# Performance work log

Measured on AMD Instinct MI355X. Metric: run time of the kernel, lower is better.

The kernel has to match this reference:

```python
import jax, jax.numpy as jnp
import numpy as np

N_FEAT = 8   # node_features_count
E_FEAT = 4   # edge_features_count
NUM_IN = 2 * (N_FEAT + 2) + E_FEAT + 1   # 25
NUM_OUT = 2 * N_FEAT + E_FEAT           # 20
E = 1048576  # number of edges (batched)


def setup_inputs() -> dict:
    key = jax.random.key(0)
    ks = jax.random.split(key, 12)
    inp = {
        "r": jax.random.uniform(ks[0], (E,), dtype=jnp.float32),
        "a_data": jax.random.normal(ks[1], (E, N_FEAT), dtype=jnp.float32),
        "a_material": jax.random.normal(ks[2], (E,), dtype=jnp.float32),
        "a_influx": jax.random.normal(ks[3], (E,), dtype=jnp.float32),
        "b_data": jax.random.normal(ks[4], (E, N_FEAT), dtype=jnp.float32),
        "b_material": jax.random.normal(ks[5], (E,), dtype=jnp.float32),
        "b_influx": jax.random.normal(ks[6], (E,), dtype=jnp.float32),
        "e_data": jax.random.normal(ks[7], (E, E_FEAT), dtype=jnp.float32),
        # Linear params, init matching torch: weight ~ N(0, 0.1), bias = 0
        "W1": 0.1 * jax.random.normal(ks[8], (NUM_IN, NUM_IN), dtype=jnp.float32),
        "b1": jnp.zeros((NUM_IN,), dtype=jnp.float32),
        "W2": 0.1 * jax.random.normal(ks[9], (NUM_OUT, NUM_IN), dtype=jnp.float32),
        "b2": jnp.zeros((NUM_OUT,), dtype=jnp.float32),
    }
    return inp


def reference(r, a_data, a_material, a_influx, b_data, b_material, b_influx,
              e_data, W1, b1, W2, b2):
    # concat per-edge features: [E, NUM_IN]
    x = jnp.concatenate(
        [r[:, None], a_data, a_material[:, None], a_influx[:, None],
         b_data, b_material[:, None], b_influx[:, None], e_data], axis=1)
    x = jax.nn.relu(x @ W1.T + b1)            # [E, NUM_IN]
    x = jax.nn.relu(x @ W2.T + b2)            # [E, NUM_OUT]
    n = N_FEAT
    return (x[:, 0:n], x[:, n:2 * n], x[:, 2 * n:])
```

## Files before the change

### kernel.cpp

```cpp
#include <hip/hip_runtime.h>
#include <cstdint>

constexpr int N_FEAT  = 8;
constexpr int E_FEAT  = 4;
constexpr int NUM_IN  = 2 * (N_FEAT + 2) + E_FEAT + 1;
constexpr int NUM_OUT = 2 * N_FEAT + E_FEAT;

__global__ __launch_bounds__(256)
__attribute__((amdgpu_waves_per_eu(4, 4)))
void edge_mlp(
    const float* __restrict__ r,
    const float* __restrict__ a_data,
    const float* __restrict__ a_mat,
    const float* __restrict__ a_inf,
    const float* __restrict__ b_data,
    const float* __restrict__ b_mat,
    const float* __restrict__ b_inf,
    const float* __restrict__ e_data,
    const float* __restrict__ W1,
    const float* __restrict__ B1,
    const float* __restrict__ W2,
    const float* __restrict__ B2,
    float*       __restrict__ out,
    int E) {
  int e = blockIdx.x * blockDim.x + threadIdx.x;
  if (e >= E) return;

  const float4* a4 = reinterpret_cast<const float4*>(a_data) + 2 * (size_t)e;
  const float4* b4 = reinterpret_cast<const float4*>(b_data) + 2 * (size_t)e;
  float4 a0 = a4[0], a1 = a4[1];
  float4 b0 = b4[0], b1v = b4[1];
  float4 ev = reinterpret_cast<const float4*>(e_data)[e];

  float x[NUM_IN];
  x[0]  = r[e];
  x[1]  = a0.x; x[2]  = a0.y; x[3]  = a0.z; x[4]  = a0.w;
  x[5]  = a1.x; x[6]  = a1.y; x[7]  = a1.z; x[8]  = a1.w;
  x[9]  = a_mat[e];
  x[10] = a_inf[e];
  x[11] = b0.x; x[12] = b0.y; x[13] = b0.z; x[14] = b0.w;
  x[15] = b1v.x; x[16] = b1v.y; x[17] = b1v.z; x[18] = b1v.w;
  x[19] = b_mat[e];
  x[20] = b_inf[e];
  x[21] = ev.x; x[22] = ev.y; x[23] = ev.z; x[24] = ev.w;

  float h[NUM_IN];
#pragma unroll
  for (int j = 0; j < NUM_IN; ++j) {
    float acc = B1[j];
    const float* wr = W1 + j * NUM_IN;
#pragma unroll
    for (int k = 0; k < NUM_IN; ++k) acc = fmaf(wr[k], x[k], acc);
    h[j] = fmaxf(acc, 0.0f);
  }

  float y[NUM_OUT];
#pragma unroll
  for (int j = 0; j < NUM_OUT; ++j) {
    float acc = B2[j];
    const float* wr = W2 + j * NUM_IN;
#pragma unroll
    for (int k = 0; k < NUM_IN; ++k) acc = fmaf(wr[k], h[k], acc);
    y[j] = fmaxf(acc, 0.0f);
  }

  float4* o0 = reinterpret_cast<float4*>(out) + 2 * (size_t)e;
  o0[0] = make_float4(y[0], y[1], y[2],  y[3]);
  o0[1] = make_float4(y[4], y[5], y[6],  y[7]);
  float4* o1 = reinterpret_cast<float4*>(out + (size_t)8 * E) + 2 * (size_t)e;
  o1[0] = make_float4(y[8],  y[9],  y[10], y[11]);
  o1[1] = make_float4(y[12], y[13], y[14], y[15]);
  reinterpret_cast<float4*>(out + (size_t)16 * E)[e] =
      make_float4(y[16], y[17], y[18], y[19]);
}

extern "C" void kernel_launch(void* const* d_in, const int* in_sizes, int n_in,
                              void* d_out, int out_size, void* d_ws, size_t ws_size,
                              hipStream_t stream) {
  const float* r      = (const float*)d_in[0];
  const float* a_data = (const float*)d_in[1];
  const float* a_mat  = (const float*)d_in[2];
  const float* a_inf  = (const float*)d_in[3];
  const float* b_data = (const float*)d_in[4];
  const float* b_mat  = (const float*)d_in[5];
  const float* b_inf  = (const float*)d_in[6];
  const float* e_data = (const float*)d_in[7];
  const float* W1     = (const float*)d_in[8];
  const float* B1     = (const float*)d_in[9];
  const float* W2     = (const float*)d_in[10];
  const float* B2     = (const float*)d_in[11];
  int E = in_sizes[0];

  edge_mlp<<<(E + 255) / 256, 256, 0, stream>>>(
      r, a_data, a_mat, a_inf, b_data, b_mat, b_inf, e_data,
      W1, B1, W2, B2, (float*)d_out, E);
}
```

Measured before the change: 206.6 us.

## Process four edges per thread to reuse weight loads across edges

Each thread now handles four edges strided by the block size, and every weight value it loads is used in four FMAs instead of one. This cuts the scalar and constant weight-load traffic per FMA. The occupancy hint drops from 4 to 2 waves per EU to leave room for about four times the live registers. Fewer waves in flight may hide memory latency less well in what is likely a bandwidth-bound kernel.

```diff
diff --git a/kernel.cpp b/kernel.cpp
--- a/kernel.cpp
+++ b/kernel.cpp
@@ -5,9 +5,11 @@
 constexpr int E_FEAT  = 4;
 constexpr int NUM_IN  = 2 * (N_FEAT + 2) + E_FEAT + 1;
 constexpr int NUM_OUT = 2 * N_FEAT + E_FEAT;
+constexpr int M       = 4;
+constexpr int BLK     = 256;
 
-__global__ __launch_bounds__(256)
-__attribute__((amdgpu_waves_per_eu(4, 4)))
+__global__ __launch_bounds__(BLK)
+__attribute__((amdgpu_waves_per_eu(2, 2)))
 void edge_mlp(
     const float* __restrict__ r,
     const float* __restrict__ a_data,
@@ -23,55 +25,85 @@
     const float* __restrict__ B2,
     float*       __restrict__ out,
     int E) {
-  int e = blockIdx.x * blockDim.x + threadIdx.x;
-  if (e >= E) return;
+  const int tid = threadIdx.x;
+  const size_t base = (size_t)blockIdx.x * (BLK * M) + tid;
 
-  const float4* a4 = reinterpret_cast<const float4*>(a_data) + 2 * (size_t)e;
-  const float4* b4 = reinterpret_cast<const float4*>(b_data) + 2 * (size_t)e;
-  float4 a0 = a4[0], a1 = a4[1];
-  float4 b0 = b4[0], b1v = b4[1];
-  float4 ev = reinterpret_cast<const float4*>(e_data)[e];
+  float x[M][NUM_IN];
+#pragma unroll
+  for (int m = 0; m < M; ++m) {
+    size_t e = base + (size_t)m * BLK;
+    if (e < (size_t)E) {
+      const float4* a4 = reinterpret_cast<const float4*>(a_data) + 2 * e;
+      const float4* b4 = reinterpret_cast<const float4*>(b_data) + 2 * e;
+      float4 a0 = a4[0], a1 = a4[1];
+      float4 b0 = b4[0], b1v = b4[1];
+      float4 ev = reinterpret_cast<const float4*>(e_data)[e];
+      x[m][0]  = r[e];
+      x[m][1]  = a0.x;  x[m][2]  = a0.y;  x[m][3]  = a0.z;  x[m][4]  = a0.w;
+      x[m][5]  = a1.x;  x[m][6]  = a1.y;  x[m][7]  = a1.z;  x[m][8]  = a1.w;
+      x[m][9]  = a_mat[e];
+      x[m][10] = a_inf[e];
+      x[m][11] = b0.x;  x[m][12] = b0.y;  x[m][13] = b0.z;  x[m][14] = b0.w;
+      x[m][15] = b1v.x; x[m][16] = b1v.y; x[m][17] = b1v.z; x[m][18] = b1v.w;
+      x[m][19] = b_mat[e];
+      x[m][20] = b_inf[e];
+      x[m][21] = ev.x;  x[m][22] = ev.y;  x[m][23] = ev.z;  x[m][24] = ev.w;
+    } else {
+#pragma unroll
+      for (int k = 0; k < NUM_IN; ++k) x[m][k] = 0.0f;
+    }
+  }
 
-  float x[NUM_IN];
-  x[0]  = r[e];
-  x[1]  = a0.x; x[2]  = a0.y; x[3]  = a0.z; x[4]  = a0.w;
-  x[5]  = a1.x; x[6]  = a1.y; x[7]  = a1.z; x[8]  = a1.w;
-  x[9]  = a_mat[e];
-  x[10] = a_inf[e];
-  x[11] = b0.x; x[12] = b0.y; x[13] = b0.z; x[14] = b0.w;
-  x[15] = b1v.x; x[16] = b1v.y; x[17] = b1v.z; x[18] = b1v.w;
-  x[19] = b_mat[e];
-  x[20] = b_inf[e];
-  x[21] = ev.x; x[22] = ev.y; x[23] = ev.z; x[24] = ev.w;
-
-  float h[NUM_IN];
+  float h[M][NUM_IN];
 #pragma unroll
   for (int j = 0; j < NUM_IN; ++j) {
-    float acc = B1[j];
     const float* wr = W1 + j * NUM_IN;
+    float acc[M];
+    float bj = B1[j];
 #pragma unroll
-    for (int k = 0; k < NUM_IN; ++k) acc = fmaf(wr[k], x[k], acc);
-    h[j] = fmaxf(acc, 0.0f);
+    for (int m = 0; m < M; ++m) acc[m] = bj;
+#pragma unroll
+    for (int k = 0; k < NUM_IN; ++k) {
+      float wk = wr[k];
+#pragma unroll
+      for (int m = 0; m < M; ++m) acc[m] = fmaf(wk, x[m][k], acc[m]);
+    }
+#pragma unroll
+    for (int m = 0; m < M; ++m) h[m][j] = fmaxf(acc[m], 0.0f);
   }
 
-  float y[NUM_OUT];
+  float y[M][NUM_OUT];
 #pragma unroll
   for (int j = 0; j < NUM_OUT; ++j) {
-    float acc = B2[j];
     const float* wr = W2 + j * NUM_IN;
+    float acc[M];
+    float bj = B2[j];
 #pragma unroll
-    for (int k = 0; k < NUM_IN; ++k) acc = fmaf(wr[k], h[k], acc);
-    y[j] = fmaxf(acc, 0.0f);
+    for (int m = 0; m < M; ++m) acc[m] = bj;
+#pragma unroll
+    for (int k = 0; k < NUM_IN; ++k) {
+      float wk = wr[k];
+#pragma unroll
+      for (int m = 0; m < M; ++m) acc[m] = fmaf(wk, h[m][k], acc[m]);
+    }
+#pragma unroll
+    for (int m = 0; m < M; ++m) y[m][j] = fmaxf(acc[m], 0.0f);
   }
 
-  float4* o0 = reinterpret_cast<float4*>(out) + 2 * (size_t)e;
-  o0[0] = make_float4(y[0], y[1], y[2],  y[3]);
-  o0[1] = make_float4(y[4], y[5], y[6],  y[7]);
-  float4* o1 = reinterpret_cast<float4*>(out + (size_t)8 * E) + 2 * (size_t)e;
-  o1[0] = make_float4(y[8],  y[9],  y[10], y[11]);
-  o1[1] = make_float4(y[12], y[13], y[14], y[15]);
-  reinterpret_cast<float4*>(out + (size_t)16 * E)[e] =
-      make_float4(y[16], y[17], y[18], y[19]);
+#pragma unroll
+  for (int m = 0; m < M; ++m) {
+    size_t e = base + (size_t)m * BLK;
+    if (e < (size_t)E) {
+      float4* o0 = reinterpret_cast<float4*>(out) + 2 * e;
+      o0[0] = make_float4(y[m][0], y[m][1], y[m][2],  y[m][3]);
+      o0[1] = make_float4(y[m][4], y[m][5], y[m][6],  y[m][7]);
+      float4* o1 = reinterpret_cast<float4*>(out + (size_t)8 * E) + 2 * e;
+      o1[0] = make_float4(y[m][8],  y[m][9],  y[m][10], y[m][11]);
+      o1[1] = make_float4(y[m][12], y[m][13], y[m][14], y[m][15]);
+      reinterpret_cast<float4*>(out + (size_t)16 * E)[e] =
+          make_float4(y[m][16], y[m][17], y[m][18], y[m][19]);
+    }
+  }
 }
 
 extern "C" void kernel_launch(void* const* d_in, const int* in_sizes, int n_in,
@@ -91,7 +123,9 @@
   const float* B2     = (const float*)d_in[11];
   int E = in_sizes[0];
 
-  edge_mlp<<<(E + 255) / 256, 256, 0, stream>>>(
+  int edges_per_block = BLK * M;
+  int grid = (E + edges_per_block - 1) / edges_per_block;
+  edge_mlp<<<grid, BLK, 0, stream>>>(
       r, a_data, a_mat, a_inf, b_data, b_mat, b_inf, e_data,
       W1, B1, W2, B2, (float*)d_out, E);
 }
```

After: 286.2 us. 38.5% more time.
